# Optimization experiments

Hardware: AMD Instinct MI355X
Metric: run time of the kernel (lower is better)

## Reference

```python
import jax, jax.numpy as jnp
import numpy as np

EPS = 1e-6


def setup_inputs() -> dict:
    key = jax.random.key(0)
    ks = jax.random.split(key, 10)
    N1, N2, K, E, LAYERS = 4096, 4096, 10, 262144, 3
    D = 2 ** K  # 1024
    us = jax.random.uniform(ks[0], (LAYERS, N1, D), dtype=jnp.float32)
    vs = jax.random.uniform(ks[1], (LAYERS, N2, D), dtype=jnp.float32)
    gamma = jax.random.normal(ks[2], (N1, LAYERS), dtype=jnp.float32)
    delta = jax.random.normal(ks[3], (N2, LAYERS), dtype=jnp.float32)
    latent_z1 = jax.random.uniform(ks[4], (N1, LAYERS), dtype=jnp.float32)
    latent_w1 = jax.random.uniform(ks[5], (N2, LAYERS), dtype=jnp.float32)
    # p_k_l initialized as log(uniform) in torch; any real values are valid params
    p_ks = jnp.full((LAYERS, K + 1), jnp.log(1.0 / (K + 1)), dtype=jnp.float32)
    p_ks = p_ks + 0.01 * jax.random.normal(ks[6], (LAYERS, K + 1), dtype=jnp.float32)
    L_ = 5.0 * jnp.ones((1,), dtype=jnp.float32)
    sparse_is = jax.random.randint(ks[7], (LAYERS, E), 0, N1, dtype=jnp.int64) if jax.config.jax_enable_x64 else jax.random.randint(ks[7], (LAYERS, E), 0, N1).astype(jnp.int32)
    sparse_js = jax.random.randint(ks[8], (LAYERS, E), 0, N2).astype(sparse_is.dtype)
    return {"us": us, "vs": vs, "gamma": gamma, "delta": delta,
            "latent_z1": latent_z1, "latent_w1": latent_w1,
            "p_ks": p_ks, "L_": L_,
            "sparse_is": sparse_is, "sparse_js": sparse_js}


def reference(us, vs, gamma, delta, latent_z1, latent_w1, p_ks, L_, sparse_is, sparse_js):
    LAYERS, N1, D = us.shape
    N2 = vs.shape[1]
    K = p_ks.shape[1] - 1  # tree_height
    latent_z = jax.nn.softmax(latent_z1, axis=1)  # Softmax(dim=1)
    latent_w = jax.nn.softmax(latent_w1, axis=1)
    L = jax.nn.softplus(L_)[0]
    ll = jnp.float32(0.0)
    for layer in range(LAYERS):
        p_k = jax.nn.softmax(p_ks[layer], axis=0)  # soft_0
        g = gamma[:, layer]                         # [N1]
        d = delta[:, layer]                         # [N2]
        emb_z = jax.nn.softmax(us[layer], axis=1)   # [N1, D]
        emb_w = jax.nn.softmax(vs[layer], axis=1)   # [N2, D]
        # hierarchical tree-weighted similarity: sum of GEMMs at coarsening levels
        inter = p_k[0] * jnp.ones((N1, N2), dtype=us.dtype)
        z_k, w_k = emb_z, emb_w
        for k in range(1, K):
            z_k = z_k.reshape(N1, -1, 2).sum(axis=2)  # [N1, D/2^k]
            w_k = w_k.reshape(N2, -1, 2).sum(axis=2)  # [N2, D/2^k]
            inter = inter + p_k[k] * jnp.einsum('nd,md->nm', z_k, w_k + EPS)
        inter = inter + p_k[K] * jnp.einsum('nd,md->nm', emb_z, emb_w + EPS)
        mat_1 = g[:, None] + d[None, :]                              # [N1, N2]
        mat_0 = (latent_z[:, layer][:, None] * L) * (latent_w[:, layer] + EPS)[None, :] * inter
        mat = jax.nn.softplus(mat_0 + mat_1)
        z_pdist1 = mat.sum()
        if N1 == N2:  # remove diagonal contributions
            z_pdist1 = z_pdist1 - jnp.trace(mat)
        i_ = sparse_is[layer]
        j_ = sparse_js[layer]
        z_pdist2 = (mat_0[i_, j_] + mat_1[i_, j_]).sum()
        ll = ll + (z_pdist2 - z_pdist1)
    return ll
```

## Files before the change

kernel.cpp:

```cpp
#include <hip/hip_runtime.h>
#include <hip/hip_bf16.h>
#include <stdint.h>

#define EPSV 1e-6f
#define N1 4096
#define N2 4096
#define DD 1024
#define NLAYERS 3
#define KKC 10

typedef __bf16 bf16_t;
typedef __bf16 bf16x8 __attribute__((ext_vector_type(8)));
typedef float f32x4 __attribute__((ext_vector_type(4)));

#define ZSCALE 256.0f
#define WSCALE 64.0f
#define INVSCALE 6.103515625e-05f

__device__ __forceinline__ float softplus_fast(float x) {
  return fmaxf(x, 0.f) + __logf(1.f + __expf(-fabsf(x)));
}
__device__ __forceinline__ float softplus_ref(float x) {
  return fmaxf(x, 0.f) + log1pf(expf(-fabsf(x)));
}
__device__ __forceinline__ float wredsum(float x) {
  #pragma unroll
  for (int o = 32; o; o >>= 1) x += __shfl_xor(x, o, 64);
  return x;
}
__device__ __forceinline__ float wredmax(float x) {
  #pragma unroll
  for (int o = 32; o; o >>= 1) x = fmaxf(x, __shfl_xor(x, o, 64));
  return x;
}
__device__ __forceinline__ void global_load_lds16(const void* g, void* l) {
  __builtin_amdgcn_global_load_lds(
      (const __attribute__((address_space(1))) uint32_t*)g,
      (__attribute__((address_space(3))) uint32_t*)l, 16, 0, 0);
}

__device__ __forceinline__ uint32_t enc_e4m3(float x) {
  if (x < 0.015625f) return (uint32_t)__float2int_rn(x * 512.0f);
  uint32_t u = __float_as_uint(x);
  u += 0x7FFFFu + ((u >> 20) & 1u);
  return (((u >> 23) - 120u) << 3) | ((u >> 20) & 7u);
}

__global__ __launch_bounds__(256) void prep_small(
    const float* __restrict__ lz, const float* __restrict__ lw,
    const float* __restrict__ gamma, const float* __restrict__ delta,
    const float* __restrict__ pks, const float* __restrict__ Lp,
    float* __restrict__ consts, float* __restrict__ a_tab, float* __restrict__ b_tab,
    float* __restrict__ g_tab, float* __restrict__ d_tab,
    uint32_t* __restrict__ hist, float* __restrict__ out)
{
  int n = blockIdx.x * blockDim.x + threadIdx.x;
  float Lv = softplus_ref(Lp[0]);
  if (n == 0) out[0] = 0.f;
  if (n < NLAYERS*256) hist[n] = 0u;
  if (n < N1) {
    float z0 = lz[n*3], z1 = lz[n*3+1], z2 = lz[n*3+2];
    float m = fmaxf(z0, fmaxf(z1, z2));
    float e0 = expf(z0-m), e1 = expf(z1-m), e2 = expf(z2-m);
    float inv = 1.f/(e0+e1+e2);
    a_tab[0*N1+n] = e0*inv*Lv; a_tab[1*N1+n] = e1*inv*Lv; a_tab[2*N1+n] = e2*inv*Lv;
    float w0 = lw[n*3], w1 = lw[n*3+1], w2 = lw[n*3+2];
    m = fmaxf(w0, fmaxf(w1, w2));
    e0 = expf(w0-m); e1 = expf(w1-m); e2 = expf(w2-m);
    inv = 1.f/(e0+e1+e2);
    b_tab[0*N2+n] = e0*inv+EPSV; b_tab[1*N2+n] = e1*inv+EPSV; b_tab[2*N2+n] = e2*inv+EPSV;
    #pragma unroll
    for (int k = 0; k < 3; ++k) {
      g_tab[k*N1+n] = gamma[n*3+k];
      d_tab[k*N2+n] = delta[n*3+k];
    }
  }
  if (n < NLAYERS) {
    float p[KKC+1]; float m = -1e30f;
    for (int k = 0; k <= KKC; ++k) { p[k] = pks[n*(KKC+1)+k]; m = fmaxf(m, p[k]); }
    float s = 0.f;
    for (int k = 0; k <= KKC; ++k) { p[k] = expf(p[k]-m); s += p[k]; }
    float inv = 1.f/s;
    for (int k = 0; k <= KKC; ++k) consts[8 + n*(KKC+1) + k] = p[k]*inv;
    consts[n] = p[0]*inv + EPSV*(1.f - p[0]*inv);
  }
}

#define EPB 2048

__global__ __launch_bounds__(256) void edge_hist(
    const int* __restrict__ is_, const int* __restrict__ js_,
    uint32_t* __restrict__ hist, int E)
{
  __shared__ uint32_t h[256];
  const int lay = blockIdx.y;
  const int t = threadIdx.x;
  h[t] = 0u;
  __syncthreads();
  const int e0 = blockIdx.x * EPB;
  const int e1 = min(e0 + EPB, E);
  for (int e = e0 + t; e < e1; e += 256) {
    int i = is_[(size_t)lay*E + e], j = js_[(size_t)lay*E + e];
    atomicAdd(&h[(i>>8)*16 + (j>>8)], 1u);
  }
  __syncthreads();
  if (h[t]) atomicAdd(&hist[lay*256 + t], h[t]);
}

__global__ __launch_bounds__(256) void edge_scan(
    const uint32_t* __restrict__ hist, uint32_t* __restrict__ off,
    uint32_t* __restrict__ cursor)
{
  __shared__ uint32_t sa[768], sb[768];
  const int t = threadIdx.x;
  for (int i = t; i < 768; i += 256) sa[i] = hist[i];
  __syncthreads();
  uint32_t* src = sa; uint32_t* dst = sb;
  for (int s = 1; s < 768; s <<= 1) {
    for (int i = t; i < 768; i += 256) dst[i] = src[i] + (i >= s ? src[i-s] : 0u);
    __syncthreads();
    uint32_t* tmp = src; src = dst; dst = tmp;
  }
  for (int i = t; i < 768; i += 256) {
    uint32_t ex = i ? src[i-1] : 0u;
    off[i] = ex; cursor[i] = ex;
  }
  if (t == 0) off[768] = src[767];
}

__global__ __launch_bounds__(256) void edge_scatter(
    const int* __restrict__ is_, const int* __restrict__ js_,
    uint32_t* __restrict__ cursor, uint16_t* __restrict__ ebuf, int E)
{
  __shared__ uint32_t h[256];
  __shared__ uint32_t basev[256];
  const int lay = blockIdx.y;
  const int t = threadIdx.x;
  h[t] = 0u;
  __syncthreads();
  const int e0 = blockIdx.x * EPB;
  const int e1 = min(e0 + EPB, E);
  for (int e = e0 + t; e < e1; e += 256) {
    int i = is_[(size_t)lay*E + e], j = js_[(size_t)lay*E + e];
    atomicAdd(&h[(i>>8)*16 + (j>>8)], 1u);
  }
  __syncthreads();
  basev[t] = h[t] ? atomicAdd(&cursor[lay*256 + t], h[t]) : 0u;
  h[t] = 0u;
  __syncthreads();
  for (int e = e0 + t; e < e1; e += 256) {
    int i = is_[(size_t)lay*E + e], j = js_[(size_t)lay*E + e];
    int b = (i>>8)*16 + (j>>8);
    uint32_t r = atomicAdd(&h[b], 1u);
    ebuf[basev[b] + r] = (uint16_t)(((i & 255) << 8) | (j & 255));
  }
}

__global__ __launch_bounds__(256) void prep_rows(
    const float* __restrict__ us, const float* __restrict__ vs,
    uint8_t* __restrict__ zt8, uint8_t* __restrict__ wt8, size_t lstride,
    const float* __restrict__ consts, int layer0)
{
  const int t = threadIdx.x, w = t >> 6, l = t & 63;
  const int n = blockIdx.x*4 + w;
  const int layer = layer0 + blockIdx.y;
  const int zmode = (blockIdx.z == 0);
  const float* src = (zmode ? us : vs) + ((size_t)layer*N1 + n)*DD + l*16;
  uint8_t* dst = (zmode ? zt8 : wt8) + (size_t)blockIdx.y*lstride + (size_t)n*1024 + l*16;

  float e[16];
  {
    const float4* s4 = (const float4*)src;
    float4 u0 = s4[0], u1 = s4[1], u2 = s4[2], u3 = s4[3];
    e[0]=u0.x; e[1]=u0.y; e[2]=u0.z; e[3]=u0.w;
    e[4]=u1.x; e[5]=u1.y; e[6]=u1.z; e[7]=u1.w;
    e[8]=u2.x; e[9]=u2.y; e[10]=u2.z; e[11]=u2.w;
    e[12]=u3.x; e[13]=u3.y; e[14]=u3.z; e[15]=u3.w;
  }
  float mx = e[0];
  #pragma unroll
  for (int i = 1; i < 16; ++i) mx = fmaxf(mx, e[i]);
  mx = wredmax(mx);
  float s = 0.f;
  #pragma unroll
  for (int i = 0; i < 16; ++i) { e[i] = __expf(e[i]-mx); s += e[i]; }
  s = wredsum(s);
  float inv = 1.f/s;
  #pragma unroll
  for (int i = 0; i < 16; ++i) e[i] *= inv;

  uint32_t b4[4] = {0u, 0u, 0u, 0u};
  if (!zmode) {
    #pragma unroll
    for (int i = 0; i < 16; ++i)
      b4[i>>2] |= enc_e4m3(e[i]*WSCALE) << ((i&3)*8);
    *(uint4*)dst = *(uint4*)b4;
    return;
  }
  float s1[8], s2[4], s3[2], s4v;
  #pragma unroll
  for (int i = 0; i < 8; ++i) s1[i] = e[2*i] + e[2*i+1];
  #pragma unroll
  for (int i = 0; i < 4; ++i) s2[i] = s1[2*i] + s1[2*i+1];
  s3[0] = s2[0]+s2[1]; s3[1] = s2[2]+s2[3];
  s4v = s3[0]+s3[1];
  float s5 = s4v + __shfl_xor(s4v, 1, 64);
  float s6 = s5  + __shfl_xor(s5, 2, 64);
  float s7 = s6  + __shfl_xor(s6, 4, 64);
  float s8 = s7  + __shfl_xor(s7, 8, 64);
  float s9 = s8  + __shfl_xor(s8, 16, 64);
  const float* pk = consts + 8 + layer*(KKC+1);
  const float base = pk[4]*s4v + pk[5]*s5 + pk[6]*s6 + pk[7]*s7 + pk[8]*s8 + pk[9]*s9;
  const float p1 = pk[1], p2 = pk[2], p3 = pk[3], p10 = pk[10];
  #pragma unroll
  for (int i = 0; i < 16; ++i) {
    float v = p10*e[i] + p1*s1[i>>1] + p2*s2[i>>2] + p3*s3[i>>3] + base;
    b4[i>>2] |= enc_e4m3(v*ZSCALE) << ((i&3)*8);
  }
  *(uint4*)dst = *(uint4*)b4;
}

__global__ __launch_bounds__(512, 2) void gemm_fused(
    const uint8_t* __restrict__ Az8, size_t zls,
    const uint8_t* __restrict__ Bw8, size_t wls,
    const float* __restrict__ a_tab, const float* __restrict__ b_tab,
    const float* __restrict__ g_tab, const float* __restrict__ d_tab,
    const float* __restrict__ consts, int layer0,
    const uint32_t* __restrict__ eoff, const uint16_t* __restrict__ ebuf,
    float* __restrict__ out)
{
  extern __shared__ char lds[];
  const int t = threadIdx.x;
  const int w = t >> 6, l = t & 63;
  const int wm = w >> 2, wn = w & 3;
  const int fr = l & 15, fq = l >> 4;

  const int nbx = gridDim.x, nby = gridDim.y;
  int lid = blockIdx.x + nbx*(blockIdx.y + nby*blockIdx.z);
  const int nblk = nbx*nby*gridDim.z;
  const int cpx = nblk >> 3;
  int nid = (lid & 7)*cpx + (lid >> 3);
  const int bz = nid / (nbx*nby);
  const int rem = nid % (nbx*nby);
  const int bi = rem % nbx, bj = rem / nbx;

  const int i0 = bi*256, j0 = bj*256;
  const int layer = layer0 + bz;
  Az8 += (size_t)bz*zls + (size_t)i0*1024;
  Bw8 += (size_t)bz*wls + (size_t)j0*1024;

  f32x4 acc[8][4];
  f32x4 zero = {0.f, 0.f, 0.f, 0.f};
  #pragma unroll
  for (int m = 0; m < 8; ++m)
    #pragma unroll
    for (int nn = 0; nn < 4; ++nn) acc[m][nn] = zero;

  const int go = (l & 7) ^ (l >> 3);
  const size_t s_off = (size_t)((l >> 3)*2 + (go >> 2))*1024 + (size_t)(go & 3)*16;
  int aKc[2];
  #pragma unroll
  for (int kc = 0; kc < 2; ++kc)
    aKc[kc] = (fr>>1)*128 + ((((fr&1)<<2) + kc*2 + (fq>>1)) ^ (fr>>1))*16 + (fq&1)*8;

  long ar[8], br[4];

#define STG_A(tile) do { \
    char* _d = lds + ((tile)&3)*32768 + w*2048; \
    const uint8_t* _s = Az8 + (size_t)(w*32)*1024 + (size_t)(tile)*64 + s_off; \
    global_load_lds16(_s, _d); \
    global_load_lds16(_s + (size_t)16*1024, _d + 1024); \
  } while (0)
#define STG_B(tile) do { \
    char* _d = lds + ((tile)&3)*32768 + 16384 + w*2048; \
    const uint8_t* _s = Bw8 + (size_t)(w*32)*1024 + (size_t)(tile)*64 + s_off; \
    global_load_lds16(_s, _d); \
    global_load_lds16(_s + (size_t)16*1024, _d + 1024); \
  } while (0)
#define LDA(bufb, mq) do { \
    const char* _b = lds + (bufb) + wm*8192; \
    _Pragma("unroll") for (int i = 0; i < 4; ++i) \
    _Pragma("unroll") for (int kc = 0; kc < 2; ++kc) \
      ar[i*2+kc] = *(const long*)(_b + ((mq)*4+i)*1024 + aKc[kc]); \
  } while (0)
#define LDB(bufb, nq) do { \
    const char* _b = lds + (bufb) + 16384 + wn*4096; \
    _Pragma("unroll") for (int j = 0; j < 2; ++j) \
    _Pragma("unroll") for (int kc = 0; kc < 2; ++kc) \
      br[j*2+kc] = *(const long*)(_b + ((nq)*2+j)*1024 + aKc[kc]); \
  } while (0)
#define MM(mq, nq) do { \
    _Pragma("unroll") for (int kc = 0; kc < 2; ++kc) \
    _Pragma("unroll") for (int i = 0; i < 4; ++i) \
    _Pragma("unroll") for (int j = 0; j < 2; ++j) \
      acc[(mq)*4+i][(nq)*2+j] = __builtin_amdgcn_mfma_f32_16x16x32_fp8_fp8( \
          ar[i*2+kc], br[j*2+kc], acc[(mq)*4+i][(nq)*2+j], 0, 0, 0); \
  } while (0)
#define BAR() asm volatile("s_barrier" ::: "memory")
#define PRIO_MM(mq, nq) do { \
    __builtin_amdgcn_s_setprio(1); MM(mq, nq); __builtin_amdgcn_s_setprio(0); } while (0)

  STG_A(0); STG_B(0); STG_A(1); STG_B(1);
  asm volatile("s_waitcnt vmcnt(4)" ::: "memory");
  BAR();

  #pragma unroll 4
  for (int u = 0; u < 16; ++u) {
    const int cb = (u & 3)*32768;
    LDA(cb, 0); LDB(cb, 0);
    if (u < 14) STG_A(u+2);
    BAR(); PRIO_MM(0, 0);
    LDB(cb, 1);
    if (u < 14) STG_B(u+2);
    BAR(); PRIO_MM(0, 1);
    LDA(cb, 1);
    BAR(); PRIO_MM(1, 0);
    if (u < 14)       asm volatile("s_waitcnt vmcnt(4)" ::: "memory");
    else if (u == 14) asm volatile("s_waitcnt vmcnt(0)" ::: "memory");
    BAR(); PRIO_MM(1, 1);
  }
#undef STG_A
#undef STG_B
#undef LDA
#undef LDB
#undef MM
#undef BAR
#undef PRIO_MM

  const float cc = consts[layer];
  {
    char* cbase = lds + wm*65536 + fq*2048 + wn*128 + fr*2;
    #pragma unroll
    for (int m = 0; m < 8; ++m)
      #pragma unroll
      for (int nn = 0; nn < 4; ++nn)
        #pragma unroll
        for (int r = 0; r < 4; ++r)
          *(bf16_t*)(cbase + m*8192 + r*512 + nn*32) =
              (bf16_t)(acc[m][nn][r]*INVSCALE + cc);
  }
  __syncthreads();

  const float* at = a_tab + layer*N1;
  const float* bt = b_tab + layer*N2;
  const float* gt = g_tab + layer*N1;
  const float* dt = d_tab + layer*N2;
  float dsum = 0.f;
  #pragma unroll 4
  for (int i = 0; i < 16; ++i) {
    const int id = t + i*512;
    const int row = id >> 5, g = id & 31;
    bf16x8 v = *(const bf16x8*)(lds + row*512 + g*16);
    const int grow = i0 + row, gcol = j0 + g*8;
    const float av = at[grow], gv = gt[grow];
    float4 b0 = *(const float4*)(bt + gcol), b1 = *(const float4*)(bt + gcol + 4);
    float4 d0 = *(const float4*)(dt + gcol), d1 = *(const float4*)(dt + gcol + 4);
    float bb[8] = {b0.x,b0.y,b0.z,b0.w,b1.x,b1.y,b1.z,b1.w};
    float dd[8] = {d0.x,d0.y,d0.z,d0.w,d1.x,d1.y,d1.z,d1.w};
    #pragma unroll
    for (int e2 = 0; e2 < 8; ++e2) {
      float x = av*bb[e2]*(float)v[e2] + gv + dd[e2];
      float sp = softplus_fast(x);
      dsum += (grow != gcol + e2) ? sp : 0.f;
    }
  }
  const int bin = bz*256 + bi*16 + bj;
  const uint32_t e0 = eoff[bin], e1 = eoff[bin+1];
  float ssum = 0.f;
  for (uint32_t e = e0 + (uint32_t)t; e < e1; e += 512u) {
    const int pk2 = ebuf[e];
    const int li = pk2 >> 8, lj = pk2 & 255;
    float dc = (float)*(const bf16_t*)(lds + li*512 + lj*2);
    ssum += at[i0+li]*bt[j0+lj]*dc + gt[i0+li] + dt[j0+lj];
  }
  float tot = wredsum(ssum - dsum);
  __syncthreads();
  if (l == 0) ((float*)lds)[w] = tot;
  __syncthreads();
  if (t == 0) {
    const float* r = (const float*)lds;
    float s = 0.f;
    #pragma unroll
    for (int i = 0; i < 8; ++i) s += r[i];
    atomicAdd(out, s);
  }
}

extern "C" void kernel_launch(void* const* d_in, const int* in_sizes, int n_in,
                              void* d_out, int out_size, void* d_ws, size_t ws_size,
                              hipStream_t stream) {
  const float* us    = (const float*)d_in[0];
  const float* vs    = (const float*)d_in[1];
  const float* gamma = (const float*)d_in[2];
  const float* delta = (const float*)d_in[3];
  const float* lz    = (const float*)d_in[4];
  const float* lw    = (const float*)d_in[5];
  const float* pks   = (const float*)d_in[6];
  const float* Lp    = (const float*)d_in[7];
  const int*   sis   = (const int*)d_in[8];
  const int*   sjs   = (const int*)d_in[9];
  float* out = (float*)d_out;
  char*  ws  = (char*)d_ws;
  const int E = in_sizes[8] / NLAYERS;

  size_t p = 0;
  float* consts = (float*)(ws + p); p += 1024;
  float* a_tab  = (float*)(ws + p); p += (size_t)NLAYERS*N1*4;
  float* b_tab  = (float*)(ws + p); p += (size_t)NLAYERS*N2*4;
  float* g_tab  = (float*)(ws + p); p += (size_t)NLAYERS*N1*4;
  float* d_tab  = (float*)(ws + p); p += (size_t)NLAYERS*N2*4;
  uint32_t* hist   = (uint32_t*)(ws + p); p += 1024*4;
  uint32_t* eoff   = (uint32_t*)(ws + p); p += 1024*4;
  uint32_t* cursor = (uint32_t*)(ws + p); p += 1024*4;
  uint16_t* ebuf   = (uint16_t*)(ws + p); p += (size_t)NLAYERS*E*2;
  p = (p + 4095) & ~(size_t)4095;
  uint8_t* zt8 = (uint8_t*)(ws + p); p += (size_t)NLAYERS*N1*1024;
  uint8_t* wt8 = (uint8_t*)(ws + p); p += (size_t)NLAYERS*N2*1024;
  if (ws_size < p) return;
  const size_t ZLS = (size_t)N1*1024;
  const size_t LDSB = 131072;
  const int nebl = (E + EPB - 1) / EPB;

  prep_small<<<(N1+255)/256, 256, 0, stream>>>(lz, lw, gamma, delta, pks, Lp,
                                               consts, a_tab, b_tab, g_tab, d_tab,
                                               hist, out);
  edge_hist<<<dim3(nebl, NLAYERS), 256, 0, stream>>>(sis, sjs, hist, E);
  edge_scan<<<1, 256, 0, stream>>>(hist, eoff, cursor);
  edge_scatter<<<dim3(nebl, NLAYERS), 256, 0, stream>>>(sis, sjs, cursor, ebuf, E);
  prep_rows<<<dim3(N1/4, NLAYERS, 2), 256, 0, stream>>>(us, vs, zt8, wt8, ZLS, consts, 0);
  gemm_fused<<<dim3(16,16,NLAYERS), 512, LDSB, stream>>>(
      zt8, ZLS, wt8, ZLS, a_tab, b_tab, g_tab, d_tab, consts, 0, eoff, ebuf, out);
}
```

Baseline: 155.0 us.

## Permute fp8 K layout in prep so GEMM loads 16-byte LDS fragments

The prep kernel now writes each row's fp8 values in a permuted K order, so each lane's two MFMA k-chunks sit next to each other in memory. The GEMM then reads A and B fragments with one 16-byte LDS load per fragment instead of two 8-byte loads, which halves the LDS read instruction count. The MFMA order changes to run the kc pair back to back on the same accumulator, creating a dependency chain. Correctness depends on the permutation and the swizzle mapping lining up, and the permuted writes from prep are 8-byte scattered stores.

```diff
diff --git a/kernel.cpp b/kernel.cpp
--- a/kernel.cpp
+++ b/kernel.cpp
@@ -12,6 +12,7 @@
 typedef __bf16 bf16_t;
 typedef __bf16 bf16x8 __attribute__((ext_vector_type(8)));
 typedef float f32x4 __attribute__((ext_vector_type(4)));
+typedef long longx2 __attribute__((ext_vector_type(2)));
 
 #define ZSCALE 256.0f
 #define WSCALE 64.0f
@@ -166,7 +167,8 @@
   const int layer = layer0 + blockIdx.y;
   const int zmode = (blockIdx.z == 0);
   const float* src = (zmode ? us : vs) + ((size_t)layer*N1 + n)*DD + l*16;
-  uint8_t* dst = (zmode ? zt8 : wt8) + (size_t)blockIdx.y*lstride + (size_t)n*1024 + l*16;
+  uint8_t* drow = (zmode ? zt8 : wt8) + (size_t)blockIdx.y*lstride + (size_t)n*1024;
+  const int p0 = (l>>2)*64 + ((l&1)*2)*16 + ((l&3)>>1)*8;
 
   float e[16];
   {
@@ -194,30 +196,32 @@
     #pragma unroll
     for (int i = 0; i < 16; ++i)
       b4[i>>2] |= enc_e4m3(e[i]*WSCALE) << ((i&3)*8);
-    *(uint4*)dst = *(uint4*)b4;
-    return;
-  }
-  float s1[8], s2[4], s3[2], s4v;
-  #pragma unroll
-  for (int i = 0; i < 8; ++i) s1[i] = e[2*i] + e[2*i+1];
-  #pragma unroll
-  for (int i = 0; i < 4; ++i) s2[i] = s1[2*i] + s1[2*i+1];
-  s3[0] = s2[0]+s2[1]; s3[1] = s2[2]+s2[3];
-  s4v = s3[0]+s3[1];
-  float s5 = s4v + __shfl_xor(s4v, 1, 64);
-  float s6 = s5  + __shfl_xor(s5, 2, 64);
-  float s7 = s6  + __shfl_xor(s6, 4, 64);
-  float s8 = s7  + __shfl_xor(s7, 8, 64);
-  float s9 = s8  + __shfl_xor(s8, 16, 64);
-  const float* pk = consts + 8 + layer*(KKC+1);
-  const float base = pk[4]*s4v + pk[5]*s5 + pk[6]*s6 + pk[7]*s7 + pk[8]*s8 + pk[9]*s9;
-  const float p1 = pk[1], p2 = pk[2], p3 = pk[3], p10 = pk[10];
-  #pragma unroll
-  for (int i = 0; i < 16; ++i) {
-    float v = p10*e[i] + p1*s1[i>>1] + p2*s2[i>>2] + p3*s3[i>>3] + base;
-    b4[i>>2] |= enc_e4m3(v*ZSCALE) << ((i&3)*8);
-  }
-  *(uint4*)dst = *(uint4*)b4;
+  } else {
+    float s1[8], s2[4], s3[2], s4v;
+    #pragma unroll
+    for (int i = 0; i < 8; ++i) s1[i] = e[2*i] + e[2*i+1];
+    #pragma unroll
+    for (int i = 0; i < 4; ++i) s2[i] = s1[2*i] + s1[2*i+1];
+    s3[0] = s2[0]+s2[1]; s3[1] = s2[2]+s2[3];
+    s4v = s3[0]+s3[1];
+    float s5 = s4v + __shfl_xor(s4v, 1, 64);
+    float s6 = s5  + __shfl_xor(s5, 2, 64);
+    float s7 = s6  + __shfl_xor(s6, 4, 64);
+    float s8 = s7  + __shfl_xor(s7, 8, 64);
+    float s9 = s8  + __shfl_xor(s8, 16, 64);
+    const float* pk = consts + 8 + layer*(KKC+1);
+    const float base = pk[4]*s4v + pk[5]*s5 + pk[6]*s6 + pk[7]*s7 + pk[8]*s8 + pk[9]*s9;
+    const float p1 = pk[1], p2 = pk[2], p3 = pk[3], p10 = pk[10];
+    #pragma unroll
+    for (int i = 0; i < 16; ++i) {
+      float v = p10*e[i] + p1*s1[i>>1] + p2*s2[i>>2] + p3*s3[i>>3] + base;
+      b4[i>>2] |= enc_e4m3(v*ZSCALE) << ((i&3)*8);
+    }
+  }
+  uint64_t u0 = (uint64_t)b4[0] | ((uint64_t)b4[1] << 32);
+  uint64_t u1 = (uint64_t)b4[2] | ((uint64_t)b4[3] << 32);
+  *(uint64_t*)(drow + p0)      = u0;
+  *(uint64_t*)(drow + p0 + 16) = u1;
 }
 
 __global__ __launch_bounds__(512, 2) void gemm_fused(
@@ -258,12 +262,12 @@
 
   const int go = (l & 7) ^ (l >> 3);
   const size_t s_off = (size_t)((l >> 3)*2 + (go >> 2))*1024 + (size_t)(go & 3)*16;
-  int aKc[2];
-  #pragma unroll
-  for (int kc = 0; kc < 2; ++kc)
-    aKc[kc] = (fr>>1)*128 + ((((fr&1)<<2) + kc*2 + (fq>>1)) ^ (fr>>1))*16 + (fq&1)*8;
-
-  long ar[8], br[4];
+  const int sl = fr >> 1;
+  const int slot = (((fr & 1) << 2) + fq) ^ sl;
+  const int abase = wm*8192 + sl*128 + slot*16;
+  const int bbase = 16384 + wn*4096 + sl*128 + slot*16;
+
+  longx2 ar2[4], br2[4];
 
 #define STG_A(tile) do { \
     char* _d = lds + ((tile)&3)*32768 + w*2048; \
@@ -278,23 +282,22 @@
     global_load_lds16(_s + (size_t)16*1024, _d + 1024); \
   } while (0)
 #define LDA(bufb, mq) do { \
-    const char* _b = lds + (bufb) + wm*8192; \
+    const char* _b = lds + (bufb) + abase; \
     _Pragma("unroll") for (int i = 0; i < 4; ++i) \
-    _Pragma("unroll") for (int kc = 0; kc < 2; ++kc) \
-      ar[i*2+kc] = *(const long*)(_b + ((mq)*4+i)*1024 + aKc[kc]); \
+      ar2[i] = *(const longx2*)(_b + ((mq)*4+i)*1024); \
   } while (0)
 #define LDB(bufb, nq) do { \
-    const char* _b = lds + (bufb) + 16384 + wn*4096; \
+    const char* _b = lds + (bufb) + bbase; \
     _Pragma("unroll") for (int j = 0; j < 2; ++j) \
-    _Pragma("unroll") for (int kc = 0; kc < 2; ++kc) \
-      br[j*2+kc] = *(const long*)(_b + ((nq)*2+j)*1024 + aKc[kc]); \
+      br2[(nq)*2+j] = *(const longx2*)(_b + ((nq)*2+j)*1024); \
   } while (0)
 #define MM(mq, nq) do { \
-    _Pragma("unroll") for (int kc = 0; kc < 2; ++kc) \
     _Pragma("unroll") for (int i = 0; i < 4; ++i) \
-    _Pragma("unroll") for (int j = 0; j < 2; ++j) \
+    _Pragma("unroll") for (int j = 0; j < 2; ++j) { \
       acc[(mq)*4+i][(nq)*2+j] = __builtin_amdgcn_mfma_f32_16x16x32_fp8_fp8( \
-          ar[i*2+kc], br[j*2+kc], acc[(mq)*4+i][(nq)*2+j], 0, 0, 0); \
+          ar2[i].x, br2[(nq)*2+j].x, acc[(mq)*4+i][(nq)*2+j], 0, 0, 0); \
+      acc[(mq)*4+i][(nq)*2+j] = __builtin_amdgcn_mfma_f32_16x16x32_fp8_fp8( \
+          ar2[i].y, br2[(nq)*2+j].y, acc[(mq)*4+i][(nq)*2+j], 0, 0, 0); } \
   } while (0)
 #define BAR() asm volatile("s_barrier" ::: "memory")
 #define PRIO_MM(mq, nq) do { \
```

New measurement: 151.8 us. 1.02x faster.
